# Kernel optimization log

Hardware: AMD Instinct MI355X
Metric: run time of the kernel (lower is better)

The kernel has to match this reference:

```python
import jax, jax.numpy as jnp
import numpy as np

K = 5            # srn kernel size (kernels[0])
EPSILON = 1e-3   # epsilons -> SRN additive noise scale
BN_EPS = 1e-5
NUM_SLICES = 3
OUT_CH = 64
CLASSES = 5


def _unfold(x, k):
    # torch.nn.Unfold, padding=0: (B, C*k*k, L), channel-major then (kh, kw) row-major
    B, C, H, W = x.shape
    Ho, Wo = H - k + 1, W - k + 1
    cols = jnp.stack([x[:, :, i:i + Ho, j:j + Wo]
                      for i in range(k) for j in range(k)], axis=2)  # (B,C,k*k,Ho,Wo)
    return cols.reshape(B, C * k * k, Ho * Wo), Ho, Wo


def _bn(x, g, b):
    # BatchNorm2d in training mode: batch statistics, biased variance
    m = x.mean((0, 2, 3), keepdims=True)
    v = x.var((0, 2, 3), keepdims=True)
    return (x - m) * jax.lax.rsqrt(v + BN_EPS) * g[None, :, None, None] + b[None, :, None, None]


def _conv(x, w, b):
    y = jax.lax.conv_general_dilated(x, w, (1, 1), 'VALID',
                                     dimension_numbers=('NCHW', 'OIHW', 'NCHW'))
    return y + b[None, :, None, None]


def _avgpool(x, s):
    B, C, H, W = x.shape
    return x.reshape(B, C, H // s, s, W // s, s).mean((3, 5))


def _maxpool(x, s):
    B, C, H, W = x.shape
    return x.reshape(B, C, H // s, s, W // s, s).max((3, 5))


def _srn(x, srn_w):
    B = x.shape[0]
    y, Ho, Wo = _unfold(x, K)                               # (B, n, L)
    y = y + EPSILON * jax.random.normal(jax.random.key(42), y.shape, y.dtype)
    gg = jnp.std(y, axis=1, ddof=1, keepdims=True)          # torch.std is unbiased
    y = y / gg
    O, C, _, _, S = srn_w.shape
    n = C * K * K
    X = srn_w.reshape(O, n, S)
    X = jnp.concatenate([jnp.ones((O, n, 1), X.dtype), X], axis=2)   # (O, n, S+1)
    Xcov = jnp.einsum('onf,ong->ofg', X, X)                 # X^T X, (O, 4, 4)
    Xinv = jnp.linalg.inv(Xcov)
    M = jnp.einsum('ofg,ong->ofn', Xinv, X)
    Wc = jnp.einsum('ofn,bnl->bofl', M, y)
    pred = jnp.einsum('onf,bofl->bonl', X, Wc)              # fitted values (B,O,n,L)
    err = jnp.mean((y[:, None] - pred) ** 2, axis=2)        # (B,O,L)
    err = err.reshape(B, O, Ho, Wo)
    A = (jnp.exp(-err) - np.exp(-1.0)) / (1.0 - np.exp(-1.0))
    return A - 0.5


def setup_inputs() -> dict:
    key = jax.random.key(0)
    ks = jax.random.split(key, 12)
    x = jax.random.normal(ks[0], (4, 3, 64, 64), jnp.float32)
    # xavier-style init scaled up for numerical stability of the small-matrix inverse
    srn_w = 0.05 * jax.random.normal(ks[1], (OUT_CH, 3, K, K, NUM_SLICES), jnp.float32)
    conv2_w = 0.05 * jax.random.normal(ks[2], (128, 64, 3, 3), jnp.float32)
    conv2_b = 0.01 * jax.random.normal(ks[3], (128,), jnp.float32)
    conv3_w = 0.05 * jax.random.normal(ks[4], (128, 128, 3, 3), jnp.float32)
    conv3_b = 0.01 * jax.random.normal(ks[5], (128,), jnp.float32)
    conv4_w = 0.05 * jax.random.normal(ks[6], (128, 128, 3, 3), jnp.float32)
    conv4_b = 0.01 * jax.random.normal(ks[7], (128,), jnp.float32)
    bn1_g = jnp.ones((64,), jnp.float32); bn1_b = jnp.zeros((64,), jnp.float32)
    bn2_g = jnp.ones((128,), jnp.float32); bn2_b = jnp.zeros((128,), jnp.float32)
    bn3_g = jnp.ones((128,), jnp.float32); bn3_b = jnp.zeros((128,), jnp.float32)
    bn4_g = jnp.ones((128,), jnp.float32); bn4_b = jnp.zeros((128,), jnp.float32)
    fc2_w = 0.05 * jax.random.normal(ks[8], (CLASSES, 128, 1, 1), jnp.float32)
    fc2_b = 0.01 * jax.random.normal(ks[9], (CLASSES,), jnp.float32)
    return dict(x=x, srn_w=srn_w, conv2_w=conv2_w, conv2_b=conv2_b,
                conv3_w=conv3_w, conv3_b=conv3_b, conv4_w=conv4_w, conv4_b=conv4_b,
                bn1_g=bn1_g, bn1_b=bn1_b, bn2_g=bn2_g, bn2_b=bn2_b,
                bn3_g=bn3_g, bn3_b=bn3_b, bn4_g=bn4_g, bn4_b=bn4_b,
                fc2_w=fc2_w, fc2_b=fc2_b)


def reference(x, srn_w, conv2_w, conv2_b, conv3_w, conv3_b, conv4_w, conv4_b,
              bn1_g, bn1_b, bn2_g, bn2_b, bn3_g, bn3_b, bn4_g, bn4_b,
              fc2_w, fc2_b):
    h = _srn(x, srn_w)                                      # (B,64,60,60)
    h = _avgpool(h, 2)
    h = _bn(h, bn1_g, bn1_b)
    h = jax.nn.relu(_bn(_conv(h, conv2_w, conv2_b), bn2_g, bn2_b))
    h = _avgpool(h, 2)
    h = jax.nn.relu(_bn(_conv(h, conv3_w, conv3_b), bn3_g, bn3_b))
    h = _maxpool(h, 2)
    h = jax.nn.relu(_bn(_conv(h, conv4_w, conv4_b), bn4_g, bn4_b))
    h = _maxpool(h, 4)                                      # (B,128,1,1)
    flat = h.reshape(h.shape[0], -1)                        # (B,128)
    return flat @ fc2_w.reshape(CLASSES, -1).T + fc2_b      # 1x1 conv == matmul
```

## Files before the change

kernel.cpp:

```cpp
#include <hip/hip_runtime.h>
#include <math.h>

__device__ __align__(16) float g_G[64 * 16];
__device__ __align__(16) float g_Wp[64 * 240];
__device__ __align__(16) float g_w2p[9 * 2304 * 4];
__device__ __align__(16) float g_w3p[17 * 2304 * 4];
__device__ __align__(16) float g_w4p[8 * 4608 * 4];
__device__ float g_s1[64],  g_q1[64];
__device__ float g_s2[128], g_q2[128];
__device__ float g_s3[128], g_q3[128];
__device__ float g_s4[128], g_q4[128];
__device__ __align__(16) float g_h1[4 * 30 * 30 * 64];
__device__ __align__(16) float g_h2[4 * 14 * 14 * 4 * 128];
__device__ __align__(16) float g_h3[4 * 6 * 6 * 4 * 128];
__device__ __align__(16) float g_h4[4 * 16 * 128];

__global__ void k_prep(const float* __restrict__ srn_w, const float* __restrict__ w2,
                       const float* __restrict__ w3, const float* __restrict__ w4) {
    int t = threadIdx.x, bid = blockIdx.x;
    int gid = bid * 256 + t, gstride = 128 * 256;
    for (int i = gid; i < 14400; i += gstride) {
        int o = i / 225, j = i % 225, row = j / 15, col = j % 15;
        g_Wp[o * 240 + row * 16 + col] = srn_w[i];
    }
    for (int j = gid; j < 73728; j += gstride) {
        int c = j & 3, s4 = j >> 2;
        int sl = s4 % 36, tmp = s4 / 36, oc_l = tmp & 63, blk = tmp >> 6;
        int it = blk & 3, ocg = blk >> 2;
        int kw = sl % 3, icq = (sl / 3) & 3, kh = sl / 12;
        int ic = it * 16 + icq * 4 + c;
        g_w2p[j] = w2[((ocg * 64 + oc_l) * 64 + ic) * 9 + kh * 3 + kw];
    }
    for (int j = gid; j < 147456; j += gstride) {
        int c = j & 3, s4 = j >> 2;
        int sl = s4 % 36, tmp = s4 / 36, oc_l = tmp & 63, blk = tmp >> 6;
        int it = blk & 7, ocg = blk >> 3;
        int kw = sl % 3, icq = (sl / 3) & 3, kh = sl / 12;
        int ic = it * 16 + icq * 4 + c;
        g_w3p[j] = w3[((ocg * 64 + oc_l) * 128 + ic) * 9 + kh * 3 + kw];
    }
    for (int j = gid; j < 147456; j += gstride) {
        int c = j & 3, s4 = j >> 2;
        int sl = s4 % 72, tmp = s4 / 72, oc_l = tmp & 15, blkq = tmp >> 4;
        int icq = blkq & 3, ocg = blkq >> 2;
        int kw = sl % 3, icb = (sl / 3) & 7, kh = sl / 24;
        int ic = icq * 32 + icb * 4 + c;
        g_w4p[j] = w4[((ocg * 16 + oc_l) * 128 + ic) * 9 + kh * 3 + kw];
    }
    if (bid == 0) {
        if (t < 64) { g_s1[t] = 0.f; g_q1[t] = 0.f; }
        if (t < 128) {
            g_s2[t] = 0.f; g_q2[t] = 0.f;
            g_s3[t] = 0.f; g_q3[t] = 0.f;
            g_s4[t] = 0.f; g_q4[t] = 0.f;
        }
        if (t < 64) {
            int o = t;
            const float* w = srn_w + o * 225;
            float c01 = 0, c02 = 0, c03 = 0, c11 = 0, c12 = 0, c13 = 0,
                  c22 = 0, c23 = 0, c33 = 0;
            for (int n = 0; n < 75; n++) {
                float w1 = w[n * 3 + 0], w2v = w[n * 3 + 1], w3v = w[n * 3 + 2];
                c01 += w1; c02 += w2v; c03 += w3v;
                c11 += w1 * w1; c12 += w1 * w2v; c13 += w1 * w3v;
                c22 += w2v * w2v; c23 += w2v * w3v; c33 += w3v * w3v;
            }
            float A[4][8];
            A[0][0] = 75.f; A[0][1] = c01; A[0][2] = c02; A[0][3] = c03;
            A[1][0] = c01;  A[1][1] = c11; A[1][2] = c12; A[1][3] = c13;
            A[2][0] = c02;  A[2][1] = c12; A[2][2] = c22; A[2][3] = c23;
            A[3][0] = c03;  A[3][1] = c13; A[3][2] = c23; A[3][3] = c33;
            for (int i = 0; i < 4; i++)
                for (int j = 0; j < 4; j++) A[i][4 + j] = (i == j) ? 1.f : 0.f;
            for (int p = 0; p < 4; p++) {
                float ip = 1.f / A[p][p];
                for (int j = 0; j < 8; j++) A[p][j] *= ip;
                for (int i = 0; i < 4; i++) if (i != p) {
                    float f = A[i][p];
                    for (int j = 0; j < 8; j++) A[i][j] -= f * A[p][j];
                }
            }
            for (int i = 0; i < 4; i++)
                for (int j = 0; j < 4; j++) g_G[o * 16 + i * 4 + j] = A[i][4 + j];
        }
    }
}

__global__ __launch_bounds__(256) void k_srn(const float* __restrict__ x) {
    __shared__ __align__(16) float wlds[64 * 244];
    __shared__ __align__(16) float glds[64 * 20];
    __shared__ float xsm[648];
    __shared__ float part[2 * 15 * 66];
    __shared__ float redS[256], redQ[256];
    int blk = blockIdx.x;
    int b = blk / 60, rem = blk % 60, r = rem >> 1, ch = rem & 1;
    int t = threadIdx.x;

    float4 wreg[15];
#pragma unroll
    for (int k = 0; k < 15; k++) wreg[k] = ((const float4*)g_Wp)[k * 256 + t];
    float4 greg = ((const float4*)g_G)[t];
    float xr[3];
#pragma unroll
    for (int k = 0; k < 3; k++) {
        int i = t + k * 256;
        if (i < 648) {
            int c = i / 216, rm = i % 216, rr = rm / 36, col = rm % 36;
            int gc = ch * 30 + col; if (gc > 63) gc = 63;
            xr[k] = x[((b * 3 + c) * 64 + (2 * r + rr)) * 64 + gc];
        }
    }
#pragma unroll
    for (int k = 0; k < 15; k++) {
        int idx = k * 256 + t;
        *(float4*)&wlds[(idx / 60) * 244 + (idx % 60) * 4] = wreg[k];
    }
    *(float4*)&glds[(t >> 2) * 20 + (t & 3) * 4] = greg;
#pragma unroll
    for (int k = 0; k < 3; k++) { int i = t + k * 256; if (i < 648) xsm[i] = xr[k]; }
    __syncthreads();

    int w = t >> 6, o = t & 63;
    int rw = w & 1, cq = w >> 1, base = cq * 16;

    float z1[16], z2[16], z3[16], s[16], q[16];
#pragma unroll
    for (int i = 0; i < 16; i++) { z1[i] = 0; z2[i] = 0; z3[i] = 0; s[i] = 0; q[i] = 0; }

    for (int c = 0; c < 3; c++) {
#pragma unroll
        for (int kh = 0; kh < 5; kh++) {
            float xv[20];
#pragma unroll
            for (int k = 0; k < 20; k++) xv[k] = xsm[(c * 6 + rw + kh) * 36 + base + k];
            float wf[16];
            const float* wp = &wlds[o * 244 + (c * 5 + kh) * 16];
            *(float4*)&wf[0]  = *(const float4*)&wp[0];
            *(float4*)&wf[4]  = *(const float4*)&wp[4];
            *(float4*)&wf[8]  = *(const float4*)&wp[8];
            *(float4*)&wf[12] = *(const float4*)&wp[12];
#pragma unroll
            for (int kw = 0; kw < 5; kw++) {
                float w1 = wf[kw * 3], w2 = wf[kw * 3 + 1], w3 = wf[kw * 3 + 2];
#pragma unroll
                for (int i = 0; i < 16; i++) {
                    float v = xv[kw + i];
                    s[i] += v; q[i] += v * v;
                    z1[i] += w1 * v; z2[i] += w2 * v; z3[i] += w3 * v;
                }
            }
        }
    }

    float gm[16];
    {
        const float* gp = &glds[o * 20];
        *(float4*)&gm[0]  = *(const float4*)&gp[0];
        *(float4*)&gm[4]  = *(const float4*)&gp[4];
        *(float4*)&gm[8]  = *(const float4*)&gp[8];
        *(float4*)&gm[12] = *(const float4*)&gp[12];
    }
    const float C1 = 0.36787944117144233f;
    const float INV = 1.5819767068693265f;
#pragma unroll
    for (int pp = 0; pp < 8; pp++) {
        int pl = cq * 8 + pp;
        if (pl < 15) {
            float aa = 0.f;
#pragma unroll
            for (int e = 0; e < 2; e++) {
                int i = 2 * pp + e;
                float sum = s[i], sq = q[i];
                float gg2 = (sq - sum * sum * (1.f / 75.f)) * (1.f / 74.f);
                float zf[4] = { sum, z1[i], z2[i], z3[i] };
                float qf = 0.f;
#pragma unroll
                for (int f = 0; f < 4; f++) {
                    float acc = 0.f;
#pragma unroll
                    for (int h = 0; h < 4; h++) acc += gm[f * 4 + h] * zf[h];
                    qf += acc * zf[f];
                }
                float err = (sq - qf) / (75.f * gg2);
                aa += (expf(-err) - C1) * INV - 0.5f;
            }
            part[(rw * 15 + pl) * 66 + o] = 0.25f * aa;
        }
    }
    __syncthreads();

    int j = t >> 6;
    float ps = 0.f, pq = 0.f;
    for (int pl = j; pl < 15; pl += 4) {
        float v = part[pl * 66 + o] + part[(15 + pl) * 66 + o];
        g_h1[((b * 30 + r) * 30 + ch * 15 + pl) * 64 + o] = v;
        ps += v; pq += v * v;
    }
    redS[t] = ps; redQ[t] = pq;
    __syncthreads();
    if (t < 64) {
        atomicAdd(&g_s1[t], redS[t] + redS[64 + t] + redS[128 + t] + redS[192 + t]);
        atomicAdd(&g_q1[t], redQ[t] + redQ[64 + t] + redQ[128 + t] + redQ[192 + t]);
    }
}

__global__ __launch_bounds__(256) void k_conv2(const float* __restrict__ g1,
                                               const float* __restrict__ b1) {
    __shared__ __align__(16) float ws[64 * 148];
    __shared__ __align__(16) float xs[3 * 30 * 64];
    __shared__ float redS[256], redQ[256];
    int blk = blockIdx.x;
    int b = blk / 56, rem = blk % 56, oh = rem >> 1, ocg = rem & 1;
    int t = threadIdx.x;
    int oc_l = t & 63, qtr = t >> 6, owb = qtr * 7;

    {
        int icb = (t & 15) * 4;
        float4 S = *(const float4*)&g_s1[icb], Q = *(const float4*)&g_q1[icb];
        float4 G4 = *(const float4*)&g1[icb], B4 = *(const float4*)&b1[icb];
        float scv[4], shv[4];
        float mm[4] = { S.x, S.y, S.z, S.w }, qq[4] = { Q.x, Q.y, Q.z, Q.w };
        float gg[4] = { G4.x, G4.y, G4.z, G4.w }, bb[4] = { B4.x, B4.y, B4.z, B4.w };
#pragma unroll
        for (int c = 0; c < 4; c++) {
            float m = mm[c] * (1.f / 3600.f);
            float v = qq[c] * (1.f / 3600.f) - m * m;
            scv[c] = gg[c] * rsqrtf(v + 1e-5f);
            shv[c] = bb[c] - m * scv[c];
        }
        const float4* src4 = (const float4*)(g_h1 + (b * 900 + oh * 30) * 64);
        float4 xr[6];
#pragma unroll
        for (int k = 0; k < 6; k++) { int i4 = t + k * 256; if (i4 < 1440) xr[k] = src4[i4]; }
        const float4* wsrc0 = (const float4*)g_w2p;
        float4 wreg[9];
#pragma unroll
        for (int k = 0; k < 9; k++) wreg[k] = wsrc0[(ocg * 4) * 2304 + k * 256 + t];
#pragma unroll
        for (int k = 0; k < 6; k++) {
            int i4 = t + k * 256;
            if (i4 < 1440) {
                float4 v;
                v.x = xr[k].x * scv[0] + shv[0]; v.y = xr[k].y * scv[1] + shv[1];
                v.z = xr[k].z * scv[2] + shv[2]; v.w = xr[k].w * scv[3] + shv[3];
                *(float4*)&xs[i4 * 4] = v;
            }
        }
#pragma unroll
        for (int k = 0; k < 9; k++) {
            int idx = k * 256 + t;
            *(float4*)&ws[(idx / 36) * 148 + (idx % 36) * 4] = wreg[k];
        }
    }
    __syncthreads();

    float acc[7] = {0, 0, 0, 0, 0, 0, 0};
    const float4* wsrc = (const float4*)g_w2p + (ocg * 4) * 2304;
    for (int it = 0; it < 4; ++it) {
        float4 wreg[9];
        if (it < 3) {
#pragma unroll
            for (int k = 0; k < 9; k++) wreg[k] = wsrc[(it + 1) * 2304 + k * 256 + t];
        }
#pragma unroll 1
        for (int icq = 0; icq < 4; icq++) {
            int xoff = it * 16 + icq * 4;
#pragma unroll
            for (int kh = 0; kh < 3; kh++) {
                const float* wb = &ws[oc_l * 148 + (kh * 4 + icq) * 12];
                float4 w0 = *(const float4*)&wb[0];
                float4 w1 = *(const float4*)&wb[4];
                float4 w2v = *(const float4*)&wb[8];
                const float* xrow = &xs[(kh * 30 + owb) * 64 + xoff];
                float4 x0 = *(const float4*)&xrow[0];
                float4 x1 = *(const float4*)&xrow[64];
#pragma unroll
                for (int i = 0; i < 7; i++) {
                    float4 x2 = *(const float4*)&xrow[(i + 2) * 64];
                    acc[i] += w0.x * x0.x + w0.y * x0.y + w0.z * x0.z + w0.w * x0.w
                            + w1.x * x1.x + w1.y * x1.y + w1.z * x1.z + w1.w * x1.w
                            + w2v.x * x2.x + w2v.y * x2.y + w2v.z * x2.z + w2v.w * x2.w;
                    x0 = x1; x1 = x2;
                }
            }
        }
        if (it < 3) {
            __syncthreads();
#pragma unroll
            for (int k = 0; k < 9; k++) {
                int idx = k * 256 + t;
                *(float4*)&ws[(idx / 36) * 148 + (idx % 36) * 4] = wreg[k];
            }
            __syncthreads();
        }
    }
    int oc = ocg * 64 + oc_l;
    float ps = 0.f, pq = 0.f;
#pragma unroll
    for (int i = 0; i < 7; i++) {
        int ow = owb + i;
        g_h2[(((b * 14 + (oh >> 1)) * 14 + (ow >> 1)) * 4 + (oh & 1) * 2 + (ow & 1)) * 128 + oc] = acc[i];
        ps += acc[i]; pq += acc[i] * acc[i];
    }
    redS[t] = ps; redQ[t] = pq;
    __syncthreads();
    if (t < 64) {
        atomicAdd(&g_s2[ocg * 64 + t], redS[t] + redS[64 + t] + redS[128 + t] + redS[192 + t]);
        atomicAdd(&g_q2[ocg * 64 + t], redQ[t] + redQ[64 + t] + redQ[128 + t] + redQ[192 + t]);
    }
}

__global__ __launch_bounds__(256) void k_conv3(const float* __restrict__ g2,
                                               const float* __restrict__ b2) {
    __shared__ __align__(16) float ws[64 * 148];
    __shared__ __align__(16) float xs[3 * 14 * 128];
    __shared__ float redS[256], redQ[256];
    int blk = blockIdx.x;
    int b = blk / 24, rem = blk % 24, oh = rem >> 1, ocg = rem & 1;
    int t = threadIdx.x;
    int oc_l = t & 63, qtr = t >> 6, owb = qtr * 3;

    {
        int icb = (t & 31) * 4;
        float4 S = *(const float4*)&g_s2[icb], Q = *(const float4*)&g_q2[icb];
        float4 G4 = *(const float4*)&g2[icb], B4 = *(const float4*)&b2[icb];
        float scv[4], shv[4];
        float mm[4] = { S.x, S.y, S.z, S.w }, qq[4] = { Q.x, Q.y, Q.z, Q.w };
        float gg[4] = { G4.x, G4.y, G4.z, G4.w }, bb[4] = { B4.x, B4.y, B4.z, B4.w };
#pragma unroll
        for (int c = 0; c < 4; c++) {
            float m = mm[c] * (1.f / 3136.f);
            float v = qq[c] * (1.f / 3136.f) - m * m;
            scv[c] = gg[c] * rsqrtf(v + 1e-5f);
            shv[c] = bb[c] - m * scv[c];
        }
        const float4* wsrc0 = (const float4*)g_w3p;
        float4 wreg[9];
#pragma unroll
        for (int k = 0; k < 9; k++) wreg[k] = wsrc0[(ocg * 8) * 2304 + k * 256 + t];
        float4 va[6], vb[6], vc[6], vd[6];
#pragma unroll
        for (int k = 0; k < 6; k++) {
            int i4 = t + k * 256;
            if (i4 < 1344) {
                int px = (i4 >> 5) % 14, rr = i4 / 448;
                const float4* p0 = (const float4*)&g_h2[(((b * 14 + oh + rr) * 14 + px) * 4) * 128 + (i4 & 31) * 4];
                va[k] = p0[0]; vb[k] = p0[32]; vc[k] = p0[64]; vd[k] = p0[96];
            }
        }
#pragma unroll
        for (int k = 0; k < 9; k++) {
            int idx = k * 256 + t;
            *(float4*)&ws[(idx / 36) * 148 + (idx % 36) * 4] = wreg[k];
        }
#pragma unroll
        for (int k = 0; k < 6; k++) {
            int i4 = t + k * 256;
            if (i4 < 1344) {
                float4 o4;
                o4.x = 0.25f * (fmaxf(va[k].x * scv[0] + shv[0], 0.f) + fmaxf(vb[k].x * scv[0] + shv[0], 0.f)
                              + fmaxf(vc[k].x * scv[0] + shv[0], 0.f) + fmaxf(vd[k].x * scv[0] + shv[0], 0.f));
                o4.y = 0.25f * (fmaxf(va[k].y * scv[1] + shv[1], 0.f) + fmaxf(vb[k].y * scv[1] + shv[1], 0.f)
                              + fmaxf(vc[k].y * scv[1] + shv[1], 0.f) + fmaxf(vd[k].y * scv[1] + shv[1], 0.f));
                o4.z = 0.25f * (fmaxf(va[k].z * scv[2] + shv[2], 0.f) + fmaxf(vb[k].z * scv[2] + shv[2], 0.f)
                              + fmaxf(vc[k].z * scv[2] + shv[2], 0.f) + fmaxf(vd[k].z * scv[2] + shv[2], 0.f));
                o4.w = 0.25f * (fmaxf(va[k].w * scv[3] + shv[3], 0.f) + fmaxf(vb[k].w * scv[3] + shv[3], 0.f)
                              + fmaxf(vc[k].w * scv[3] + shv[3], 0.f) + fmaxf(vd[k].w * scv[3] + shv[3], 0.f));
                *(float4*)&xs[i4 * 4] = o4;
            }
        }
    }
    __syncthreads();

    float acc[3] = {0, 0, 0};
    const float4* wsrc = (const float4*)g_w3p + (ocg * 8) * 2304;
    for (int it = 0; it < 8; ++it) {
        float4 wreg[9];
        if (it < 7) {
#pragma unroll
            for (int k = 0; k < 9; k++) wreg[k] = wsrc[(it + 1) * 2304 + k * 256 + t];
        }
#pragma unroll 1
        for (int icq = 0; icq < 4; icq++) {
            int xoff = it * 16 + icq * 4;
#pragma unroll
            for (int kh = 0; kh < 3; kh++) {
                const float* wb = &ws[oc_l * 148 + (kh * 4 + icq) * 12];
                float4 w0 = *(const float4*)&wb[0];
                float4 w1 = *(const float4*)&wb[4];
                float4 w2v = *(const float4*)&wb[8];
                const float* xrow = &xs[(kh * 14 + owb) * 128 + xoff];
                float4 x0 = *(const float4*)&xrow[0];
                float4 x1 = *(const float4*)&xrow[128];
#pragma unroll
                for (int i = 0; i < 3; i++) {
                    float4 x2 = *(const float4*)&xrow[(i + 2) * 128];
                    acc[i] += w0.x * x0.x + w0.y * x0.y + w0.z * x0.z + w0.w * x0.w
                            + w1.x * x1.x + w1.y * x1.y + w1.z * x1.z + w1.w * x1.w
                            + w2v.x * x2.x + w2v.y * x2.y + w2v.z * x2.z + w2v.w * x2.w;
                    x0 = x1; x1 = x2;
                }
            }
        }
        if (it < 7) {
            __syncthreads();
#pragma unroll
            for (int k = 0; k < 9; k++) {
                int idx = k * 256 + t;
                *(float4*)&ws[(idx / 36) * 148 + (idx % 36) * 4] = wreg[k];
            }
            __syncthreads();
        }
    }
    int oc = ocg * 64 + oc_l;
    float ps = 0.f, pq = 0.f;
#pragma unroll
    for (int i = 0; i < 3; i++) {
        int ow = owb + i;
        g_h3[(((b * 6 + (oh >> 1)) * 6 + (ow >> 1)) * 4 + (oh & 1) * 2 + (ow & 1)) * 128 + oc] = acc[i];
        ps += acc[i]; pq += acc[i] * acc[i];
    }
    redS[t] = ps; redQ[t] = pq;
    __syncthreads();
    if (t < 64) {
        atomicAdd(&g_s3[ocg * 64 + t], redS[t] + redS[64 + t] + redS[128 + t] + redS[192 + t]);
        atomicAdd(&g_q3[ocg * 64 + t], redQ[t] + redQ[64 + t] + redQ[128 + t] + redQ[192 + t]);
    }
}

__global__ __launch_bounds__(256) void k_conv4(const float* __restrict__ g3,
                                               const float* __restrict__ b3) {
    __shared__ __align__(16) float ws[64 * 292];
    __shared__ __align__(16) float xs[3 * 6 * 128];
    __shared__ float red[256];
    int blk = blockIdx.x;
    int b = blk / 32, rem = blk % 32, oh = rem / 8, ocg = rem % 8;
    int t = threadIdx.x;
    int oc_l = t & 15, ow = (t >> 4) & 3, icq = t >> 6;

    {
        int icb = (t & 31) * 4;
        float4 S = *(const float4*)&g_s3[icb], Q = *(const float4*)&g_q3[icb];
        float4 G4 = *(const float4*)&g3[icb], B4 = *(const float4*)&b3[icb];
        float scv[4], shv[4];
        float mm[4] = { S.x, S.y, S.z, S.w }, qq[4] = { Q.x, Q.y, Q.z, Q.w };
        float gg[4] = { G4.x, G4.y, G4.z, G4.w }, bb[4] = { B4.x, B4.y, B4.z, B4.w };
#pragma unroll
        for (int c = 0; c < 4; c++) {
            float m = mm[c] * (1.f / 576.f);
            float v = qq[c] * (1.f / 576.f) - m * m;
            scv[c] = gg[c] * rsqrtf(v + 1e-5f);
            shv[c] = bb[c] - m * scv[c];
        }
        const float4* wsrc = (const float4*)g_w4p + ocg * 4608;
        float4 wreg[18];
#pragma unroll
        for (int k = 0; k < 18; k++) wreg[k] = wsrc[k * 256 + t];
        float4 va[3], vb[3], vc[3], vd[3];
#pragma unroll
        for (int k = 0; k < 3; k++) {
            int i4 = t + k * 256;
            if (i4 < 576) {
                int px = (i4 >> 5) % 6, rr = i4 / 192;
                const float4* p0 = (const float4*)&g_h3[(((b * 6 + oh + rr) * 6 + px) * 4) * 128 + (i4 & 31) * 4];
                va[k] = p0[0]; vb[k] = p0[32]; vc[k] = p0[64]; vd[k] = p0[96];
            }
        }
#pragma unroll
        for (int k = 0; k < 18; k++) {
            int idx = k * 256 + t;
            *(float4*)&ws[(idx / 72) * 292 + (idx % 72) * 4] = wreg[k];
        }
#pragma unroll
        for (int k = 0; k < 3; k++) {
            int i4 = t + k * 256;
            if (i4 < 576) {
                float4 o4;
                o4.x = fmaxf(fmaxf(fmaxf(va[k].x * scv[0] + shv[0], vb[k].x * scv[0] + shv[0]),
                                   fmaxf(vc[k].x * scv[0] + shv[0], vd[k].x * scv[0] + shv[0])), 0.f);
                o4.y = fmaxf(fmaxf(fmaxf(va[k].y * scv[1] + shv[1], vb[k].y * scv[1] + shv[1]),
                                   fmaxf(vc[k].y * scv[1] + shv[1], vd[k].y * scv[1] + shv[1])), 0.f);
                o4.z = fmaxf(fmaxf(fmaxf(va[k].z * scv[2] + shv[2], vb[k].z * scv[2] + shv[2]),
                                   fmaxf(vc[k].z * scv[2] + shv[2], vd[k].z * scv[2] + shv[2])), 0.f);
                o4.w = fmaxf(fmaxf(fmaxf(va[k].w * scv[3] + shv[3], vb[k].w * scv[3] + shv[3]),
                                   fmaxf(vc[k].w * scv[3] + shv[3], vd[k].w * scv[3] + shv[3])), 0.f);
                *(float4*)&xs[i4 * 4] = o4;
            }
        }
    }
    __syncthreads();

    float acc = 0.f;
    const float* wbase = &ws[(icq * 16 + oc_l) * 292];
#pragma unroll 1
    for (int icbq = 0; icbq < 8; icbq++) {
#pragma unroll
        for (int kh = 0; kh < 3; kh++) {
            const float* wb = &wbase[(kh * 8 + icbq) * 12];
            float4 w0 = *(const float4*)&wb[0];
            float4 w1 = *(const float4*)&wb[4];
            float4 w2v = *(const float4*)&wb[8];
            float4 x0 = *(const float4*)&xs[(kh * 6 + ow) * 128 + icq * 32 + icbq * 4];
            float4 x1 = *(const float4*)&xs[(kh * 6 + ow + 1) * 128 + icq * 32 + icbq * 4];
            float4 x2 = *(const float4*)&xs[(kh * 6 + ow + 2) * 128 + icq * 32 + icbq * 4];
            acc += w0.x * x0.x + w0.y * x0.y + w0.z * x0.z + w0.w * x0.w
                 + w1.x * x1.x + w1.y * x1.y + w1.z * x1.z + w1.w * x1.w
                 + w2v.x * x2.x + w2v.y * x2.y + w2v.z * x2.z + w2v.w * x2.w;
        }
    }
    red[t] = acc;
    __syncthreads();
    if (t < 64) {
        float v = red[t] + red[t + 64] + red[t + 128] + red[t + 192];
        int oc = ocg * 16 + (t & 15);
        g_h4[((b * 4 + oh) * 4 + (t >> 4)) * 128 + oc] = v;
        float ps = v + __shfl_xor(v, 16);  ps += __shfl_xor(ps, 32);
        float pv = v * v;
        float pq = pv + __shfl_xor(pv, 16); pq += __shfl_xor(pq, 32);
        if (t < 16) { atomicAdd(&g_s4[ocg * 16 + t], ps); atomicAdd(&g_q4[ocg * 16 + t], pq); }
    }
}

__global__ __launch_bounds__(256) void k_final(const float* __restrict__ g4,
                                               const float* __restrict__ b4,
                                               const float* __restrict__ fcw,
                                               const float* __restrict__ fcb,
                                               float* __restrict__ out) {
    __shared__ float sc[128], sh[128];
    __shared__ float pooled[4][128];
    int t = threadIdx.x;
    if (t < 128) {
        float m = g_s4[t] * (1.f / 64.f);
        float v = g_q4[t] * (1.f / 64.f) - m * m;
        float rs = rsqrtf(v + 1e-5f);
        sc[t] = g4[t] * rs; sh[t] = b4[t] - m * sc[t];
    }
    __syncthreads();
    for (int item = t; item < 512; item += 256) {
        int b = item >> 7, oc = item & 127;
        float s = sc[oc], h = sh[oc];
        float mx = 0.f;
#pragma unroll
        for (int k = 0; k < 16; k++) mx = fmaxf(mx, g_h4[(b * 16 + k) * 128 + oc] * s + h);
        pooled[b][oc] = mx;
    }
    __syncthreads();
    if (t < 20) {
        int b = t / 5, cls = t % 5;
        float acc = fcb[cls];
        const float* w = &fcw[cls * 128];
        for (int oc = 0; oc < 128; oc++) acc += pooled[b][oc] * w[oc];
        out[b * 5 + cls] = acc;
    }
}

extern "C" void kernel_launch(void* const* d_in, const int* in_sizes, int n_in,
                              void* d_out, int out_size, void* d_ws, size_t ws_size,
                              hipStream_t stream) {
    (void)in_sizes; (void)n_in; (void)out_size; (void)d_ws; (void)ws_size;
    const float* x     = (const float*)d_in[0];
    const float* srn_w = (const float*)d_in[1];
    const float* w2    = (const float*)d_in[2];
    const float* w3    = (const float*)d_in[4];
    const float* w4    = (const float*)d_in[6];
    const float* g1 = (const float*)d_in[8];  const float* b1 = (const float*)d_in[9];
    const float* g2 = (const float*)d_in[10]; const float* b2 = (const float*)d_in[11];
    const float* g3 = (const float*)d_in[12]; const float* b3 = (const float*)d_in[13];
    const float* g4 = (const float*)d_in[14]; const float* b4 = (const float*)d_in[15];
    const float* fcw = (const float*)d_in[16]; const float* fcb = (const float*)d_in[17];
    float* out = (float*)d_out;

    k_prep <<<dim3(128), dim3(256), 0, stream>>>(srn_w, w2, w3, w4);
    k_srn  <<<dim3(240), dim3(256), 0, stream>>>(x);
    k_conv2<<<dim3(224), dim3(256), 0, stream>>>(g1, b1);
    k_conv3<<<dim3(96),  dim3(256), 0, stream>>>(g2, b2);
    k_conv4<<<dim3(128), dim3(256), 0, stream>>>(g3, b3);
    k_final<<<dim3(1),   dim3(256), 0, stream>>>(g4, b4, fcw, fcb, out);
}
```

Baseline: 115.4 us.

## Fuse all stages into one persistent kernel with software grid barriers

Replaces the six separate launches (prep, srn, conv2, conv3, conv4, final) with a single persistent kernel of 240 blocks that separates the stages with an atomic-counter grid barrier. The SRN stage now streams weights one input channel at a time through a smaller LDS buffer so shared memory fits the fused kernel's dynamic allocation. The aim is to remove kernel launch gaps and tail effects between small stages. In exchange, each barrier adds a global atomic round trip. Correctness depends on all 240 blocks being co-resident, and the stages that use fewer blocks leave the rest idle at the barrier.

```diff
diff --git a/kernel.cpp b/kernel.cpp
--- a/kernel.cpp
+++ b/kernel.cpp
@@ -1,5 +1,7 @@
 #include <hip/hip_runtime.h>
 #include <math.h>
+
+#define GRID 240
 
 __device__ __align__(16) float g_G[64 * 16];
 __device__ __align__(16) float g_Wp[64 * 240];
@@ -14,47 +16,77 @@
 __device__ __align__(16) float g_h2[4 * 14 * 14 * 4 * 128];
 __device__ __align__(16) float g_h3[4 * 6 * 6 * 4 * 128];
 __device__ __align__(16) float g_h4[4 * 16 * 128];
-
-__global__ void k_prep(const float* __restrict__ srn_w, const float* __restrict__ w2,
-                       const float* __restrict__ w3, const float* __restrict__ w4) {
-    int t = threadIdx.x, bid = blockIdx.x;
-    int gid = bid * 256 + t, gstride = 128 * 256;
-    for (int i = gid; i < 14400; i += gstride) {
-        int o = i / 225, j = i % 225, row = j / 15, col = j % 15;
-        g_Wp[o * 240 + row * 16 + col] = srn_w[i];
+__device__ int g_cnt;
+__device__ int g_gen;
+
+__device__ __forceinline__ void gridbar() {
+    __syncthreads();
+    __threadfence();
+    if (threadIdx.x == 0) {
+        int gen = __hip_atomic_load(&g_gen, __ATOMIC_RELAXED, __HIP_MEMORY_SCOPE_AGENT);
+        if (__hip_atomic_fetch_add(&g_cnt, 1, __ATOMIC_ACQ_REL, __HIP_MEMORY_SCOPE_AGENT)
+            == (int)gridDim.x - 1) {
+            __hip_atomic_store(&g_cnt, 0, __ATOMIC_RELAXED, __HIP_MEMORY_SCOPE_AGENT);
+            __hip_atomic_store(&g_gen, gen + 1, __ATOMIC_RELEASE, __HIP_MEMORY_SCOPE_AGENT);
+        } else {
+            while (__hip_atomic_load(&g_gen, __ATOMIC_RELAXED, __HIP_MEMORY_SCOPE_AGENT) == gen)
+                __builtin_amdgcn_s_sleep(2);
+        }
     }
-    for (int j = gid; j < 73728; j += gstride) {
-        int c = j & 3, s4 = j >> 2;
-        int sl = s4 % 36, tmp = s4 / 36, oc_l = tmp & 63, blk = tmp >> 6;
-        int it = blk & 3, ocg = blk >> 2;
-        int kw = sl % 3, icq = (sl / 3) & 3, kh = sl / 12;
-        int ic = it * 16 + icq * 4 + c;
-        g_w2p[j] = w2[((ocg * 64 + oc_l) * 64 + ic) * 9 + kh * 3 + kw];
-    }
-    for (int j = gid; j < 147456; j += gstride) {
-        int c = j & 3, s4 = j >> 2;
-        int sl = s4 % 36, tmp = s4 / 36, oc_l = tmp & 63, blk = tmp >> 6;
-        int it = blk & 7, ocg = blk >> 3;
-        int kw = sl % 3, icq = (sl / 3) & 3, kh = sl / 12;
-        int ic = it * 16 + icq * 4 + c;
-        g_w3p[j] = w3[((ocg * 64 + oc_l) * 128 + ic) * 9 + kh * 3 + kw];
-    }
-    for (int j = gid; j < 147456; j += gstride) {
-        int c = j & 3, s4 = j >> 2;
-        int sl = s4 % 72, tmp = s4 / 72, oc_l = tmp & 15, blkq = tmp >> 4;
-        int icq = blkq & 3, ocg = blkq >> 2;
-        int kw = sl % 3, icb = (sl / 3) & 7, kh = sl / 24;
-        int ic = icq * 32 + icb * 4 + c;
-        g_w4p[j] = w4[((ocg * 16 + oc_l) * 128 + ic) * 9 + kh * 3 + kw];
-    }
-    if (bid == 0) {
-        if (t < 64) { g_s1[t] = 0.f; g_q1[t] = 0.f; }
-        if (t < 128) {
+    __syncthreads();
+    __threadfence();
+}
+
+extern "C" __global__ void __launch_bounds__(256)
+k_fused(const float* __restrict__ x, const float* __restrict__ srn_w,
+        const float* __restrict__ w2, const float* __restrict__ w3,
+        const float* __restrict__ w4,
+        const float* __restrict__ g1, const float* __restrict__ b1,
+        const float* __restrict__ g2, const float* __restrict__ b2,
+        const float* __restrict__ g3, const float* __restrict__ b3,
+        const float* __restrict__ g4, const float* __restrict__ b4,
+        const float* __restrict__ fcw, const float* __restrict__ fcb,
+        float* __restrict__ out) {
+    extern __shared__ __align__(16) float smem[];
+    int bid = blockIdx.x, t = threadIdx.x;
+
+    {
+        int gid = bid * 256 + t, gstride = GRID * 256;
+        for (int i = gid; i < 14400; i += gstride) {
+            int o = i / 225, j = i % 225, row = j / 15, col = j % 15;
+            g_Wp[o * 240 + row * 16 + col] = srn_w[i];
+        }
+        for (int j = gid; j < 73728; j += gstride) {
+            int c = j & 3, s4 = j >> 2;
+            int sl = s4 % 36, tmp = s4 / 36, oc_l = tmp & 63, blk = tmp >> 6;
+            int it = blk & 3, ocg = blk >> 2;
+            int kw = sl % 3, icq = (sl / 3) & 3, kh = sl / 12;
+            int ic = it * 16 + icq * 4 + c;
+            g_w2p[j] = w2[((ocg * 64 + oc_l) * 64 + ic) * 9 + kh * 3 + kw];
+        }
+        for (int j = gid; j < 147456; j += gstride) {
+            int c = j & 3, s4 = j >> 2;
+            int sl = s4 % 36, tmp = s4 / 36, oc_l = tmp & 63, blk = tmp >> 6;
+            int it = blk & 7, ocg = blk >> 3;
+            int kw = sl % 3, icq = (sl / 3) & 3, kh = sl / 12;
+            int ic = it * 16 + icq * 4 + c;
+            g_w3p[j] = w3[((ocg * 64 + oc_l) * 128 + ic) * 9 + kh * 3 + kw];
+        }
+        for (int j = gid; j < 147456; j += gstride) {
+            int c = j & 3, s4 = j >> 2;
+            int sl = s4 % 72, tmp = s4 / 72, oc_l = tmp & 15, blkq = tmp >> 4;
+            int icq = blkq & 3, ocg = blkq >> 2;
+            int kw = sl % 3, icb = (sl / 3) & 7, kh = sl / 24;
+            int ic = icq * 32 + icb * 4 + c;
+            g_w4p[j] = w4[((ocg * 16 + oc_l) * 128 + ic) * 9 + kh * 3 + kw];
+        }
+        if (bid == 1 && t < 128) {
+            if (t < 64) { g_s1[t] = 0.f; g_q1[t] = 0.f; }
             g_s2[t] = 0.f; g_q2[t] = 0.f;
             g_s3[t] = 0.f; g_q3[t] = 0.f;
             g_s4[t] = 0.f; g_q4[t] = 0.f;
         }
-        if (t < 64) {
+        if (bid == 0 && t < 64) {
             int o = t;
             const float* w = srn_w + o * 225;
             float c01 = 0, c02 = 0, c03 = 0, c11 = 0, c12 = 0, c13 = 0,
@@ -84,473 +116,490 @@
                 for (int j = 0; j < 4; j++) g_G[o * 16 + i * 4 + j] = A[i][4 + j];
         }
     }
-}
-
-__global__ __launch_bounds__(256) void k_srn(const float* __restrict__ x) {
-    __shared__ __align__(16) float wlds[64 * 244];
-    __shared__ __align__(16) float glds[64 * 20];
-    __shared__ float xsm[648];
-    __shared__ float part[2 * 15 * 66];
-    __shared__ float redS[256], redQ[256];
-    int blk = blockIdx.x;
-    int b = blk / 60, rem = blk % 60, r = rem >> 1, ch = rem & 1;
-    int t = threadIdx.x;
-
-    float4 wreg[15];
-#pragma unroll
-    for (int k = 0; k < 15; k++) wreg[k] = ((const float4*)g_Wp)[k * 256 + t];
-    float4 greg = ((const float4*)g_G)[t];
-    float xr[3];
-#pragma unroll
-    for (int k = 0; k < 3; k++) {
-        int i = t + k * 256;
-        if (i < 648) {
-            int c = i / 216, rm = i % 216, rr = rm / 36, col = rm % 36;
-            int gc = ch * 30 + col; if (gc > 63) gc = 63;
-            xr[k] = x[((b * 3 + c) * 64 + (2 * r + rr)) * 64 + gc];
+    gridbar();
+
+    {
+        float* wl   = smem;
+        float* gl   = smem + 5376;
+        float* xsm  = smem + 6656;
+        float* part = smem + 7304;
+        float* redS = smem + 9284;
+        float* redQ = smem + 9540;
+        int b = bid / 60, rem = bid % 60, r = rem >> 1, ch = rem & 1;
+
+        float4 greg = ((const float4*)g_G)[t];
+        float xr[3];
+#pragma unroll
+        for (int k = 0; k < 3; k++) {
+            int i = t + k * 256;
+            if (i < 648) {
+                int c = i / 216, rm = i % 216, rr = rm / 36, col = rm % 36;
+                int gc = ch * 30 + col; if (gc > 63) gc = 63;
+                xr[k] = x[((b * 3 + c) * 64 + (2 * r + rr)) * 64 + gc];
+            }
+        }
+        float4 wreg[5];
+#pragma unroll
+        for (int k = 0; k < 5; k++) {
+            int idx = k * 256 + t;
+            wreg[k] = ((const float4*)g_Wp)[(idx / 20) * 60 + 0 * 20 + (idx % 20)];
+        }
+        *(float4*)&gl[(t >> 2) * 20 + (t & 3) * 4] = greg;
+#pragma unroll
+        for (int k = 0; k < 3; k++) { int i = t + k * 256; if (i < 648) xsm[i] = xr[k]; }
+#pragma unroll
+        for (int k = 0; k < 5; k++) {
+            int idx = k * 256 + t;
+            *(float4*)&wl[(idx / 20) * 84 + (idx % 20) * 4] = wreg[k];
+        }
+        __syncthreads();
+
+        int w = t >> 6, o = t & 63;
+        int rw = w & 1, cq = w >> 1, base = cq * 16;
+
+        float z1[16], z2[16], z3[16], s[16], q[16];
+#pragma unroll
+        for (int i = 0; i < 16; i++) { z1[i]=0; z2[i]=0; z3[i]=0; s[i]=0; q[i]=0; }
+
+        for (int c = 0; c < 3; c++) {
+            if (c < 2) {
+#pragma unroll
+                for (int k = 0; k < 5; k++) {
+                    int idx = k * 256 + t;
+                    wreg[k] = ((const float4*)g_Wp)[(idx / 20) * 60 + (c + 1) * 20 + (idx % 20)];
+                }
+            }
+#pragma unroll
+            for (int kh = 0; kh < 5; kh++) {
+                float xv[20];
+#pragma unroll
+                for (int k = 0; k < 20; k++) xv[k] = xsm[(c * 6 + rw + kh) * 36 + base + k];
+                float wf[16];
+                const float* wp = &wl[o * 84 + kh * 16];
+                *(float4*)&wf[0]  = *(const float4*)&wp[0];
+                *(float4*)&wf[4]  = *(const float4*)&wp[4];
+                *(float4*)&wf[8]  = *(const float4*)&wp[8];
+                *(float4*)&wf[12] = *(const float4*)&wp[12];
+#pragma unroll
+                for (int kw = 0; kw < 5; kw++) {
+                    float w1 = wf[kw * 3], w2v = wf[kw * 3 + 1], w3v = wf[kw * 3 + 2];
+#pragma unroll
+                    for (int i = 0; i < 16; i++) {
+                        float v = xv[kw + i];
+                        s[i] += v; q[i] += v * v;
+                        z1[i] += w1 * v; z2[i] += w2v * v; z3[i] += w3v * v;
+                    }
+                }
+            }
+            if (c < 2) {
+                __syncthreads();
+#pragma unroll
+                for (int k = 0; k < 5; k++) {
+                    int idx = k * 256 + t;
+                    *(float4*)&wl[(idx / 20) * 84 + (idx % 20) * 4] = wreg[k];
+                }
+                __syncthreads();
+            }
+        }
+
+        float gm[16];
+        {
+            const float* gp = &gl[o * 20];
+            *(float4*)&gm[0]  = *(const float4*)&gp[0];
+            *(float4*)&gm[4]  = *(const float4*)&gp[4];
+            *(float4*)&gm[8]  = *(const float4*)&gp[8];
+            *(float4*)&gm[12] = *(const float4*)&gp[12];
+        }
+        const float C1 = 0.36787944117144233f;
+        const float INV = 1.5819767068693265f;
+#pragma unroll
+        for (int pp = 0; pp < 8; pp++) {
+            int pl = cq * 8 + pp;
+            if (pl < 15) {
+                float aa = 0.f;
+#pragma unroll
+                for (int e = 0; e < 2; e++) {
+                    int i = 2 * pp + e;
+                    float sum = s[i], sq = q[i];
+                    float gg2 = (sq - sum * sum * (1.f / 75.f)) * (1.f / 74.f);
+                    float zf[4] = { sum, z1[i], z2[i], z3[i] };
+                    float qf = 0.f;
+#pragma unroll
+                    for (int f = 0; f < 4; f++) {
+                        float acc = 0.f;
+#pragma unroll
+                        for (int h = 0; h < 4; h++) acc += gm[f * 4 + h] * zf[h];
+                        qf += acc * zf[f];
+                    }
+                    float err = (sq - qf) / (75.f * gg2);
+                    aa += (expf(-err) - C1) * INV - 0.5f;
+                }
+                part[(rw * 15 + pl) * 66 + o] = 0.25f * aa;
+            }
+        }
+        __syncthreads();
+
+        int j = t >> 6;
+        float ps = 0.f, pq = 0.f;
+        for (int pl = j; pl < 15; pl += 4) {
+            float v = part[pl * 66 + o] + part[(15 + pl) * 66 + o];
+            g_h1[((b * 30 + r) * 30 + ch * 15 + pl) * 64 + o] = v;
+            ps += v; pq += v * v;
+        }
+        redS[t] = ps; redQ[t] = pq;
+        __syncthreads();
+        if (t < 64) {
+            atomicAdd(&g_s1[t], redS[t] + redS[64 + t] + redS[128 + t] + redS[192 + t]);
+            atomicAdd(&g_q1[t], redQ[t] + redQ[64 + t] + redQ[128 + t] + redQ[192 + t]);
         }
     }
-#pragma unroll
-    for (int k = 0; k < 15; k++) {
-        int idx = k * 256 + t;
-        *(float4*)&wlds[(idx / 60) * 244 + (idx % 60) * 4] = wreg[k];
-    }
-    *(float4*)&glds[(t >> 2) * 20 + (t & 3) * 4] = greg;
-#pragma unroll
-    for (int k = 0; k < 3; k++) { int i = t + k * 256; if (i < 648) xsm[i] = xr[k]; }
-    __syncthreads();
-
-    int w = t >> 6, o = t & 63;
-    int rw = w & 1, cq = w >> 1, base = cq * 16;
-
-    float z1[16], z2[16], z3[16], s[16], q[16];
-#pragma unroll
-    for (int i = 0; i < 16; i++) { z1[i] = 0; z2[i] = 0; z3[i] = 0; s[i] = 0; q[i] = 0; }
-
-    for (int c = 0; c < 3; c++) {
-#pragma unroll
-        for (int kh = 0; kh < 5; kh++) {
-            float xv[20];
-#pragma unroll
-            for (int k = 0; k < 20; k++) xv[k] = xsm[(c * 6 + rw + kh) * 36 + base + k];
-            float wf[16];
-            const float* wp = &wlds[o * 244 + (c * 5 + kh) * 16];
-            *(float4*)&wf[0]  = *(const float4*)&wp[0];
-            *(float4*)&wf[4]  = *(const float4*)&wp[4];
-            *(float4*)&wf[8]  = *(const float4*)&wp[8];
-            *(float4*)&wf[12] = *(const float4*)&wp[12];
-#pragma unroll
-            for (int kw = 0; kw < 5; kw++) {
-                float w1 = wf[kw * 3], w2 = wf[kw * 3 + 1], w3 = wf[kw * 3 + 2];
-#pragma unroll
-                for (int i = 0; i < 16; i++) {
-                    float v = xv[kw + i];
-                    s[i] += v; q[i] += v * v;
-                    z1[i] += w1 * v; z2[i] += w2 * v; z3[i] += w3 * v;
-                }
-            }
-        }
-    }
-
-    float gm[16];
-    {
-        const float* gp = &glds[o * 20];
-        *(float4*)&gm[0]  = *(const float4*)&gp[0];
-        *(float4*)&gm[4]  = *(const float4*)&gp[4];
-        *(float4*)&gm[8]  = *(const float4*)&gp[8];
-        *(float4*)&gm[12] = *(const float4*)&gp[12];
-    }
-    const float C1 = 0.36787944117144233f;
-    const float INV = 1.5819767068693265f;
-#pragma unroll
-    for (int pp = 0; pp < 8; pp++) {
-        int pl = cq * 8 + pp;
-        if (pl < 15) {
-            float aa = 0.f;
-#pragma unroll
-            for (int e = 0; e < 2; e++) {
-                int i = 2 * pp + e;
-                float sum = s[i], sq = q[i];
-                float gg2 = (sq - sum * sum * (1.f / 75.f)) * (1.f / 74.f);
-                float zf[4] = { sum, z1[i], z2[i], z3[i] };
-                float qf = 0.f;
-#pragma unroll
-                for (int f = 0; f < 4; f++) {
-                    float acc = 0.f;
-#pragma unroll
-                    for (int h = 0; h < 4; h++) acc += gm[f * 4 + h] * zf[h];
-                    qf += acc * zf[f];
-                }
-                float err = (sq - qf) / (75.f * gg2);
-                aa += (expf(-err) - C1) * INV - 0.5f;
-            }
-            part[(rw * 15 + pl) * 66 + o] = 0.25f * aa;
-        }
-    }
-    __syncthreads();
-
-    int j = t >> 6;
-    float ps = 0.f, pq = 0.f;
-    for (int pl = j; pl < 15; pl += 4) {
-        float v = part[pl * 66 + o] + part[(15 + pl) * 66 + o];
-        g_h1[((b * 30 + r) * 30 + ch * 15 + pl) * 64 + o] = v;
-        ps += v; pq += v * v;
-    }
-    redS[t] = ps; redQ[t] = pq;
-    __syncthreads();
-    if (t < 64) {
-        atomicAdd(&g_s1[t], redS[t] + redS[64 + t] + redS[128 + t] + redS[192 + t]);
-        atomicAdd(&g_q1[t], redQ[t] + redQ[64 + t] + redQ[128 + t] + redQ[192 + t]);
-    }
-}
-
-__global__ __launch_bounds__(256) void k_conv2(const float* __restrict__ g1,
-                                               const float* __restrict__ b1) {
-    __shared__ __align__(16) float ws[64 * 148];
-    __shared__ __align__(16) float xs[3 * 30 * 64];
-    __shared__ float redS[256], redQ[256];
-    int blk = blockIdx.x;
-    int b = blk / 56, rem = blk % 56, oh = rem >> 1, ocg = rem & 1;
-    int t = threadIdx.x;
-    int oc_l = t & 63, qtr = t >> 6, owb = qtr * 7;
-
-    {
-        int icb = (t & 15) * 4;
-        float4 S = *(const float4*)&g_s1[icb], Q = *(const float4*)&g_q1[icb];
-        float4 G4 = *(const float4*)&g1[icb], B4 = *(const float4*)&b1[icb];
-        float scv[4], shv[4];
-        float mm[4] = { S.x, S.y, S.z, S.w }, qq[4] = { Q.x, Q.y, Q.z, Q.w };
-        float gg[4] = { G4.x, G4.y, G4.z, G4.w }, bb[4] = { B4.x, B4.y, B4.z, B4.w };
-#pragma unroll
-        for (int c = 0; c < 4; c++) {
-            float m = mm[c] * (1.f / 3600.f);
-            float v = qq[c] * (1.f / 3600.f) - m * m;
-            scv[c] = gg[c] * rsqrtf(v + 1e-5f);
-            shv[c] = bb[c] - m * scv[c];
-        }
-        const float4* src4 = (const float4*)(g_h1 + (b * 900 + oh * 30) * 64);
-        float4 xr[6];
-#pragma unroll
-        for (int k = 0; k < 6; k++) { int i4 = t + k * 256; if (i4 < 1440) xr[k] = src4[i4]; }
-        const float4* wsrc0 = (const float4*)g_w2p;
-        float4 wreg[9];
-#pragma unroll
-        for (int k = 0; k < 9; k++) wreg[k] = wsrc0[(ocg * 4) * 2304 + k * 256 + t];
-#pragma unroll
-        for (int k = 0; k < 6; k++) {
-            int i4 = t + k * 256;
-            if (i4 < 1440) {
-                float4 v;
-                v.x = xr[k].x * scv[0] + shv[0]; v.y = xr[k].y * scv[1] + shv[1];
-                v.z = xr[k].z * scv[2] + shv[2]; v.w = xr[k].w * scv[3] + shv[3];
-                *(float4*)&xs[i4 * 4] = v;
-            }
-        }
-#pragma unroll
-        for (int k = 0; k < 9; k++) {
-            int idx = k * 256 + t;
-            *(float4*)&ws[(idx / 36) * 148 + (idx % 36) * 4] = wreg[k];
-        }
-    }
-    __syncthreads();
-
-    float acc[7] = {0, 0, 0, 0, 0, 0, 0};
-    const float4* wsrc = (const float4*)g_w2p + (ocg * 4) * 2304;
-    for (int it = 0; it < 4; ++it) {
-        float4 wreg[9];
-        if (it < 3) {
-#pragma unroll
-            for (int k = 0; k < 9; k++) wreg[k] = wsrc[(it + 1) * 2304 + k * 256 + t];
-        }
-#pragma unroll 1
-        for (int icq = 0; icq < 4; icq++) {
-            int xoff = it * 16 + icq * 4;
-#pragma unroll
-            for (int kh = 0; kh < 3; kh++) {
-                const float* wb = &ws[oc_l * 148 + (kh * 4 + icq) * 12];
-                float4 w0 = *(const float4*)&wb[0];
-                float4 w1 = *(const float4*)&wb[4];
-                float4 w2v = *(const float4*)&wb[8];
-                const float* xrow = &xs[(kh * 30 + owb) * 64 + xoff];
-                float4 x0 = *(const float4*)&xrow[0];
-                float4 x1 = *(const float4*)&xrow[64];
-#pragma unroll
-                for (int i = 0; i < 7; i++) {
-                    float4 x2 = *(const float4*)&xrow[(i + 2) * 64];
-                    acc[i] += w0.x * x0.x + w0.y * x0.y + w0.z * x0.z + w0.w * x0.w
-                            + w1.x * x1.x + w1.y * x1.y + w1.z * x1.z + w1.w * x1.w
-                            + w2v.x * x2.x + w2v.y * x2.y + w2v.z * x2.z + w2v.w * x2.w;
-                    x0 = x1; x1 = x2;
-                }
-            }
-        }
-        if (it < 3) {
-            __syncthreads();
+    gridbar();
+
+    if (bid < 224) {
+        float* ws   = smem;
+        float* xs   = smem + 9472;
+        float* redS = smem + 15232;
+        float* redQ = smem + 15488;
+        int b = bid / 56, rem = bid % 56, oh = rem >> 1, ocg = rem & 1;
+        int oc_l = t & 63, qtr = t >> 6, owb = qtr * 7;
+
+        {
+            int icb = (t & 15) * 4;
+            float4 S = *(const float4*)&g_s1[icb], Q = *(const float4*)&g_q1[icb];
+            float4 G4 = *(const float4*)&g1[icb], B4 = *(const float4*)&b1[icb];
+            float scv[4], shv[4];
+            float mm[4] = { S.x, S.y, S.z, S.w }, qq[4] = { Q.x, Q.y, Q.z, Q.w };
+            float gg[4] = { G4.x, G4.y, G4.z, G4.w }, bb[4] = { B4.x, B4.y, B4.z, B4.w };
+#pragma unroll
+            for (int c = 0; c < 4; c++) {
+                float m = mm[c] * (1.f / 3600.f);
+                float v = qq[c] * (1.f / 3600.f) - m * m;
+                scv[c] = gg[c] * rsqrtf(v + 1e-5f);
+                shv[c] = bb[c] - m * scv[c];
+            }
+            const float4* src4 = (const float4*)(g_h1 + (b * 900 + oh * 30) * 64);
+            float4 xr[6];
+#pragma unroll
+            for (int k = 0; k < 6; k++) { int i4 = t + k * 256; if (i4 < 1440) xr[k] = src4[i4]; }
+            const float4* wsrc0 = (const float4*)g_w2p;
+            float4 wreg[9];
+#pragma unroll
+            for (int k = 0; k < 9; k++) wreg[k] = wsrc0[(ocg * 4) * 2304 + k * 256 + t];
+#pragma unroll
+            for (int k = 0; k < 6; k++) {
+                int i4 = t + k * 256;
+                if (i4 < 1440) {
+                    float4 v;
+                    v.x = xr[k].x * scv[0] + shv[0]; v.y = xr[k].y * scv[1] + shv[1];
+                    v.z = xr[k].z * scv[2] + shv[2]; v.w = xr[k].w * scv[3] + shv[3];
+                    *(float4*)&xs[i4 * 4] = v;
+                }
+            }
 #pragma unroll
             for (int k = 0; k < 9; k++) {
                 int idx = k * 256 + t;
                 *(float4*)&ws[(idx / 36) * 148 + (idx % 36) * 4] = wreg[k];
             }
-            __syncthreads();
+        }
+        __syncthreads();
+
+        float acc[7] = {0, 0, 0, 0, 0, 0, 0};
+        const float4* wsrc = (const float4*)g_w2p + (ocg * 4) * 2304;
+        for (int it = 0; it < 4; ++it) {
+            float4 wreg[9];
+            if (it < 3) {
+#pragma unroll
+                for (int k = 0; k < 9; k++) wreg[k] = wsrc[(it + 1) * 2304 + k * 256 + t];
+            }
+#pragma unroll 1
+            for (int icq = 0; icq < 4; icq++) {
+                int xoff = it * 16 + icq * 4;
+#pragma unroll
+                for (int kh = 0; kh < 3; kh++) {
+                    const float* wb = &ws[oc_l * 148 + (kh * 4 + icq) * 12];
+                    float4 w0 = *(const float4*)&wb[0];
+                    float4 w1 = *(const float4*)&wb[4];
+                    float4 w2v = *(const float4*)&wb[8];
+                    const float* xrow = &xs[(kh * 30 + owb) * 64 + xoff];
+                    float4 x0 = *(const float4*)&xrow[0];
+                    float4 x1 = *(const float4*)&xrow[64];
+#pragma unroll
+                    for (int i = 0; i < 7; i++) {
+                        float4 x2 = *(const float4*)&xrow[(i + 2) * 64];
+                        acc[i] += w0.x * x0.x + w0.y * x0.y + w0.z * x0.z + w0.w * x0.w
+                                + w1.x * x1.x + w1.y * x1.y + w1.z * x1.z + w1.w * x1.w
+                                + w2v.x * x2.x + w2v.y * x2.y + w2v.z * x2.z + w2v.w * x2.w;
+                        x0 = x1; x1 = x2;
+                    }
+                }
+            }
+            if (it < 3) {
+                __syncthreads();
+#pragma unroll
+                for (int k = 0; k < 9; k++) {
+                    int idx = k * 256 + t;
+                    *(float4*)&ws[(idx / 36) * 148 + (idx % 36) * 4] = wreg[k];
+                }
+                __syncthreads();
+            }
+        }
+        int oc = ocg * 64 + oc_l;
+        float ps = 0.f, pq = 0.f;
+#pragma unroll
+        for (int i = 0; i < 7; i++) {
+            int ow = owb + i;
+            g_h2[(((b * 14 + (oh >> 1)) * 14 + (ow >> 1)) * 4 + (oh & 1) * 2 + (ow & 1)) * 128 + oc] = acc[i];
+            ps += acc[i]; pq += acc[i] * acc[i];
+        }
+        redS[t] = ps; redQ[t] = pq;
+        __syncthreads();
+        if (t < 64) {
+            atomicAdd(&g_s2[ocg * 64 + t], redS[t] + redS[64 + t] + redS[128 + t] + redS[192 + t]);
+            atomicAdd(&g_q2[ocg * 64 + t], redQ[t] + redQ[64 + t] + redQ[128 + t] + redQ[192 + t]);
         }
     }
-    int oc = ocg * 64 + oc_l;
-    float ps = 0.f, pq = 0.f;
-#pragma unroll
-    for (int i = 0; i < 7; i++) {
-        int ow = owb + i;
-        g_h2[(((b * 14 + (oh >> 1)) * 14 + (ow >> 1)) * 4 + (oh & 1) * 2 + (ow & 1)) * 128 + oc] = acc[i];
-        ps += acc[i]; pq += acc[i] * acc[i];
-    }
-    redS[t] = ps; redQ[t] = pq;
-    __syncthreads();
-    if (t < 64) {
-        atomicAdd(&g_s2[ocg * 64 + t], redS[t] + redS[64 + t] + redS[128 + t] + redS[192 + t]);
-        atomicAdd(&g_q2[ocg * 64 + t], redQ[t] + redQ[64 + t] + redQ[128 + t] + redQ[192 + t]);
-    }
-}
-
-__global__ __launch_bounds__(256) void k_conv3(const float* __restrict__ g2,
-                                               const float* __restrict__ b2) {
-    __shared__ __align__(16) float ws[64 * 148];
-    __shared__ __align__(16) float xs[3 * 14 * 128];
-    __shared__ float redS[256], redQ[256];
-    int blk = blockIdx.x;
-    int b = blk / 24, rem = blk % 24, oh = rem >> 1, ocg = rem & 1;
-    int t = threadIdx.x;
-    int oc_l = t & 63, qtr = t >> 6, owb = qtr * 3;
-
-    {
-        int icb = (t & 31) * 4;
-        float4 S = *(const float4*)&g_s2[icb], Q = *(const float4*)&g_q2[icb];
-        float4 G4 = *(const float4*)&g2[icb], B4 = *(const float4*)&b2[icb];
-        float scv[4], shv[4];
-        float mm[4] = { S.x, S.y, S.z, S.w }, qq[4] = { Q.x, Q.y, Q.z, Q.w };
-        float gg[4] = { G4.x, G4.y, G4.z, G4.w }, bb[4] = { B4.x, B4.y, B4.z, B4.w };
-#pragma unroll
-        for (int c = 0; c < 4; c++) {
-            float m = mm[c] * (1.f / 3136.f);
-            float v = qq[c] * (1.f / 3136.f) - m * m;
-            scv[c] = gg[c] * rsqrtf(v + 1e-5f);
-            shv[c] = bb[c] - m * scv[c];
-        }
-        const float4* wsrc0 = (const float4*)g_w3p;
-        float4 wreg[9];
-#pragma unroll
-        for (int k = 0; k < 9; k++) wreg[k] = wsrc0[(ocg * 8) * 2304 + k * 256 + t];
-        float4 va[6], vb[6], vc[6], vd[6];
-#pragma unroll
-        for (int k = 0; k < 6; k++) {
-            int i4 = t + k * 256;
-            if (i4 < 1344) {
-                int px = (i4 >> 5) % 14, rr = i4 / 448;
-                const float4* p0 = (const float4*)&g_h2[(((b * 14 + oh + rr) * 14 + px) * 4) * 128 + (i4 & 31) * 4];
-                va[k] = p0[0]; vb[k] = p0[32]; vc[k] = p0[64]; vd[k] = p0[96];
-            }
-        }
-#pragma unroll
-        for (int k = 0; k < 9; k++) {
-            int idx = k * 256 + t;
-            *(float4*)&ws[(idx / 36) * 148 + (idx % 36) * 4] = wreg[k];
-        }
-#pragma unroll
-        for (int k = 0; k < 6; k++) {
-            int i4 = t + k * 256;
-            if (i4 < 1344) {
-                float4 o4;
-                o4.x = 0.25f * (fmaxf(va[k].x * scv[0] + shv[0], 0.f) + fmaxf(vb[k].x * scv[0] + shv[0], 0.f)
-                              + fmaxf(vc[k].x * scv[0] + shv[0], 0.f) + fmaxf(vd[k].x * scv[0] + shv[0], 0.f));
-                o4.y = 0.25f * (fmaxf(va[k].y * scv[1] + shv[1], 0.f) + fmaxf(vb[k].y * scv[1] + shv[1], 0.f)
-                              + fmaxf(vc[k].y * scv[1] + shv[1], 0.f) + fmaxf(vd[k].y * scv[1] + shv[1], 0.f));
-                o4.z = 0.25f * (fmaxf(va[k].z * scv[2] + shv[2], 0.f) + fmaxf(vb[k].z * scv[2] + shv[2], 0.f)
-                              + fmaxf(vc[k].z * scv[2] + shv[2], 0.f) + fmaxf(vd[k].z * scv[2] + shv[2], 0.f));
-                o4.w = 0.25f * (fmaxf(va[k].w * scv[3] + shv[3], 0.f) + fmaxf(vb[k].w * scv[3] + shv[3], 0.f)
-                              + fmaxf(vc[k].w * scv[3] + shv[3], 0.f) + fmaxf(vd[k].w * scv[3] + shv[3], 0.f));
-                *(float4*)&xs[i4 * 4] = o4;
-            }
-        }
-    }
-    __syncthreads();
-
-    float acc[3] = {0, 0, 0};
-    const float4* wsrc = (const float4*)g_w3p + (ocg * 8) * 2304;
-    for (int it = 0; it < 8; ++it) {
-        float4 wreg[9];
-        if (it < 7) {
-#pragma unroll
-            for (int k = 0; k < 9; k++) wreg[k] = wsrc[(it + 1) * 2304 + k * 256 + t];
-        }
-#pragma unroll 1
-        for (int icq = 0; icq < 4; icq++) {
-            int xoff = it * 16 + icq * 4;
-#pragma unroll
-            for (int kh = 0; kh < 3; kh++) {
-                const float* wb = &ws[oc_l * 148 + (kh * 4 + icq) * 12];
-                float4 w0 = *(const float4*)&wb[0];
-                float4 w1 = *(const float4*)&wb[4];
-                float4 w2v = *(const float4*)&wb[8];
-                const float* xrow = &xs[(kh * 14 + owb) * 128 + xoff];
-                float4 x0 = *(const float4*)&xrow[0];
-                float4 x1 = *(const float4*)&xrow[128];
-#pragma unroll
-                for (int i = 0; i < 3; i++) {
-                    float4 x2 = *(const float4*)&xrow[(i + 2) * 128];
-                    acc[i] += w0.x * x0.x + w0.y * x0.y + w0.z * x0.z + w0.w * x0.w
-                            + w1.x * x1.x + w1.y * x1.y + w1.z * x1.z + w1.w * x1.w
-                            + w2v.x * x2.x + w2v.y * x2.y + w2v.z * x2.z + w2v.w * x2.w;
-                    x0 = x1; x1 = x2;
-                }
-            }
-        }
-        if (it < 7) {
-            __syncthreads();
+    gridbar();
+
+    if (bid < 96) {
+        float* ws   = smem;
+        float* xs   = smem + 9472;
+        float* redS = smem + 14848;
+        float* redQ = smem + 15104;
+        int b = bid / 24, rem = bid % 24, oh = rem >> 1, ocg = rem & 1;
+        int oc_l = t & 63, qtr = t >> 6, owb = qtr * 3;
+
+        {
+            int icb = (t & 31) * 4;
+            float4 S = *(const float4*)&g_s2[icb], Q = *(const float4*)&g_q2[icb];
+            float4 G4 = *(const float4*)&g2[icb], B4 = *(const float4*)&b2[icb];
+            float scv[4], shv[4];
+            float mm[4] = { S.x, S.y, S.z, S.w }, qq[4] = { Q.x, Q.y, Q.z, Q.w };
+            float gg[4] = { G4.x, G4.y, G4.z, G4.w }, bb[4] = { B4.x, B4.y, B4.z, B4.w };
+#pragma unroll
+            for (int c = 0; c < 4; c++) {
+                float m = mm[c] * (1.f / 3136.f);
+                float v = qq[c] * (1.f / 3136.f) - m * m;
+                scv[c] = gg[c] * rsqrtf(v + 1e-5f);
+                shv[c] = bb[c] - m * scv[c];
+            }
+            const float4* wsrc0 = (const float4*)g_w3p;
+            float4 wreg[9];
+#pragma unroll
+            for (int k = 0; k < 9; k++) wreg[k] = wsrc0[(ocg * 8) * 2304 + k * 256 + t];
+            float4 pa[6], pb[6], pc[6], pd[6];
+#pragma unroll
+            for (int k = 0; k < 6; k++) {
+                int i4 = t + k * 256;
+                if (i4 < 1344) {
+                    int px = (i4 >> 5) % 14, rr = i4 / 448;
+                    const float4* p0 = (const float4*)&g_h2[(((b * 14 + oh + rr) * 14 + px) * 4) * 128 + (i4 & 31) * 4];
+                    pa[k] = p0[0]; pb[k] = p0[32]; pc[k] = p0[64]; pd[k] = p0[96];
+                }
+            }
 #pragma unroll
             for (int k = 0; k < 9; k++) {
                 int idx = k * 256 + t;
                 *(float4*)&ws[(idx / 36) * 148 + (idx % 36) * 4] = wreg[k];
             }
+#pragma unroll
+            for (int k = 0; k < 6; k++) {
+                int i4 = t + k * 256;
+                if (i4 < 1344) {
+                    float4 o4;
+                    o4.x = 0.25f * (fmaxf(pa[k].x * scv[0] + shv[0], 0.f) + fmaxf(pb[k].x * scv[0] + shv[0], 0.f)
+                                  + fmaxf(pc[k].x * scv[0] + shv[0], 0.f) + fmaxf(pd[k].x * scv[0] + shv[0], 0.f));
+                    o4.y = 0.25f * (fmaxf(pa[k].y * scv[1] + shv[1], 0.f) + fmaxf(pb[k].y * scv[1] + shv[1], 0.f)
+                                  + fmaxf(pc[k].y * scv[1] + shv[1], 0.f) + fmaxf(pd[k].y * scv[1] + shv[1], 0.f));
+                    o4.z = 0.25f * (fmaxf(pa[k].z * scv[2] + shv[2], 0.f) + fmaxf(pb[k].z * scv[2] + shv[2], 0.f)
+                                  + fmaxf(pc[k].z * scv[2] + shv[2], 0.f) + fmaxf(pd[k].z * scv[2] + shv[2], 0.f));
+                    o4.w = 0.25f * (fmaxf(pa[k].w * scv[3] + shv[3], 0.f) + fmaxf(pb[k].w * scv[3] + shv[3], 0.f)
+                                  + fmaxf(pc[k].w * scv[3] + shv[3], 0.f) + fmaxf(pd[k].w * scv[3] + shv[3], 0.f));
+                    *(float4*)&xs[i4 * 4] = o4;
+                }
+            }
+        }
+        __syncthreads();
+
+        float acc[3] = {0, 0, 0};
+        const float4* wsrc = (const float4*)g_w3p + (ocg * 8) * 2304;
+        for (int it = 0; it < 8; ++it) {
+            float4 wreg[9];
+            if (it < 7) {
+#pragma unroll
+                for (int k = 0; k < 9; k++) wreg[k] = wsrc[(it + 1) * 2304 + k * 256 + t];
+            }
+#pragma unroll 1
+            for (int icq = 0; icq < 4; icq++) {
+                int xoff = it * 16 + icq * 4;
+#pragma unroll
+                for (int kh = 0; kh < 3; kh++) {
+                    const float* wb = &ws[oc_l * 148 + (kh * 4 + icq) * 12];
+                    float4 w0 = *(const float4*)&wb[0];
+                    float4 w1 = *(const float4*)&wb[4];
+                    float4 w2v = *(const float4*)&wb[8];
+                    const float* xrow = &xs[(kh * 14 + owb) * 128 + xoff];
+                    float4 x0 = *(const float4*)&xrow[0];
+                    float4 x1 = *(const float4*)&xrow[128];
+#pragma unroll
+                    for (int i = 0; i < 3; i++) {
+                        float4 x2 = *(const float4*)&xrow[(i + 2) * 128];
+                        acc[i] += w0.x * x0.x + w0.y * x0.y + w0.z * x0.z + w0.w * x0.w
+                                + w1.x * x1.x + w1.y * x1.y + w1.z * x1.z + w1.w * x1.w
+                                + w2v.x * x2.x + w2v.y * x2.y + w2v.z * x2.z + w2v.w * x2.w;
+                        x0 = x1; x1 = x2;
+                    }
+                }
+            }
+            if (it < 7) {
+                __syncthreads();
+#pragma unroll
+                for (int k = 0; k < 9; k++) {
+                    int idx = k * 256 + t;
+                    *(float4*)&ws[(idx / 36) * 148 + (idx % 36) * 4] = wreg[k];
+                }
+                __syncthreads();
+            }
+        }
+        int oc = ocg * 64 + oc_l;
+        float ps = 0.f, pq = 0.f;
+#pragma unroll
+        for (int i = 0; i < 3; i++) {
+            int ow = owb + i;
+            g_h3[(((b * 6 + (oh >> 1)) * 6 + (ow >> 1)) * 4 + (oh & 1) * 2 + (ow & 1)) * 128 + oc] = acc[i];
+            ps += acc[i]; pq += acc[i] * acc[i];
+        }
+        redS[t] = ps; redQ[t] = pq;
+        __syncthreads();
+        if (t < 64) {
+            atomicAdd(&g_s3[ocg * 64 + t], redS[t] + redS[64 + t] + redS[128 + t] + redS[192 + t]);
+            atomicAdd(&g_q3[ocg * 64 + t], redQ[t] + redQ[64 + t] + redQ[128 + t] + redQ[192 + t]);
+        }
+    }
+    gridbar();
+
+    if (bid < 128) {
+        float* ws  = smem;
+        float* xs  = smem + 9344;
+        float* red = smem + 11648;
+        int b = bid / 32, rem = bid % 32, oh = rem / 8, ocg = rem % 8;
+        int oc_l = t & 15, ow = (t >> 4) & 3, icq = t >> 6;
+
+        {
+            int icb = (t & 31) * 4;
+            float4 S = *(const float4*)&g_s3[icb], Q = *(const float4*)&g_q3[icb];
+            float4 G4 = *(const float4*)&g3[icb], B4 = *(const float4*)&b3[icb];
+            float scv[4], shv[4];
+            float mm[4] = { S.x, S.y, S.z, S.w }, qq[4] = { Q.x, Q.y, Q.z, Q.w };
+            float gg[4] = { G4.x, G4.y, G4.z, G4.w }, bb[4] = { B4.x, B4.y, B4.z, B4.w };
+#pragma unroll
+            for (int c = 0; c < 4; c++) {
+                float m = mm[c] * (1.f / 576.f);
+                float v = qq[c] * (1.f / 576.f) - m * m;
+                scv[c] = gg[c] * rsqrtf(v + 1e-5f);
+                shv[c] = bb[c] - m * scv[c];
+            }
+            float4 pa[3], pb[3], pc[3], pd[3];
+#pragma unroll
+            for (int k = 0; k < 3; k++) {
+                int i4 = t + k * 256;
+                if (i4 < 576) {
+                    int px = (i4 >> 5) % 6, rr = i4 / 192;
+                    const float4* p0 = (const float4*)&g_h3[(((b * 6 + oh + rr) * 6 + px) * 4) * 128 + (i4 & 31) * 4];
+                    pa[k] = p0[0]; pb[k] = p0[32]; pc[k] = p0[64]; pd[k] = p0[96];
+                }
+            }
+#pragma unroll
+            for (int k = 0; k < 3; k++) {
+                int i4 = t + k * 256;
+                if (i4 < 576) {
+                    float4 o4;
+                    o4.x = fmaxf(fmaxf(fmaxf(pa[k].x * scv[0] + shv[0], pb[k].x * scv[0] + shv[0]),
+                                       fmaxf(pc[k].x * scv[0] + shv[0], pd[k].x * scv[0] + shv[0])), 0.f);
+                    o4.y = fmaxf(fmaxf(fmaxf(pa[k].y * scv[1] + shv[1], pb[k].y * scv[1] + shv[1]),
+                                       fmaxf(pc[k].y * scv[1] + shv[1], pd[k].y * scv[1] + shv[1])), 0.f);
+                    o4.z = fmaxf(fmaxf(fmaxf(pa[k].z * scv[2] + shv[2], pb[k].z * scv[2] + shv[2]),
+                                       fmaxf(pc[k].z * scv[2] + shv[2], pd[k].z * scv[2] + shv[2])), 0.f);
+                    o4.w = fmaxf(fmaxf(fmaxf(pa[k].w * scv[3] + shv[3], pb[k].w * scv[3] + shv[3]),
+                                       fmaxf(pc[k].w * scv[3] + shv[3], pd[k].w * scv[3] + shv[3])), 0.f);
+                    *(float4*)&xs[i4 * 4] = o4;
+                }
+            }
+        }
+
+        float acc = 0.f;
+        const float4* wsrc = (const float4*)g_w4p + ocg * 4608;
+        for (int h = 0; h < 2; h++) {
+            float4 wreg[9];
+#pragma unroll
+            for (int k = 0; k < 9; k++) wreg[k] = wsrc[h * 2304 + k * 256 + t];
             __syncthreads();
+#pragma unroll
+            for (int k = 0; k < 9; k++) {
+                int idx = k * 256 + t;
+                *(float4*)&ws[(idx / 72) * 292 + (idx % 72) * 4] = wreg[k];
+            }
+            __syncthreads();
+            if ((icq >> 1) == h) {
+                const float* wbase = &ws[((icq & 1) * 16 + oc_l) * 292];
+#pragma unroll 1
+                for (int icbq = 0; icbq < 8; icbq++) {
+#pragma unroll
+                    for (int kh = 0; kh < 3; kh++) {
+                        const float* wb = &wbase[(kh * 8 + icbq) * 12];
+                        float4 w0 = *(const float4*)&wb[0];
+                        float4 w1 = *(const float4*)&wb[4];
+                        float4 w2v = *(const float4*)&wb[8];
+                        float4 x0 = *(const float4*)&xs[(kh * 6 + ow) * 128 + icq * 32 + icbq * 4];
+                        float4 x1 = *(const float4*)&xs[(kh * 6 + ow + 1) * 128 + icq * 32 + icbq * 4];
+                        float4 x2 = *(const float4*)&xs[(kh * 6 + ow + 2) * 128 + icq * 32 + icbq * 4];
+                        acc += w0.x * x0.x + w0.y * x0.y + w0.z * x0.z + w0.w * x0.w
+                             + w1.x * x1.x + w1.y * x1.y + w1.z * x1.z + w1.w * x1.w
+                             + w2v.x * x2.x + w2v.y * x2.y + w2v.z * x2.z + w2v.w * x2.w;
+                    }
+                }
+            }
+        }
+        red[t] = acc;
+        __syncthreads();
+        if (t < 64) {
+            float v = red[t] + red[t + 64] + red[t + 128] + red[t + 192];
+            int oc = ocg * 16 + (t & 15);
+            g_h4[((b * 4 + oh) * 4 + (t >> 4)) * 128 + oc] = v;
+            float ps = v + __shfl_xor(v, 16);  ps += __shfl_xor(ps, 32);
+            float pv = v * v;
+            float pq = pv + __shfl_xor(pv, 16); pq += __shfl_xor(pq, 32);
+            if (t < 16) { atomicAdd(&g_s4[ocg * 16 + t], ps); atomicAdd(&g_q4[ocg * 16 + t], pq); }
         }
     }
-    int oc = ocg * 64 + oc_l;
-    float ps = 0.f, pq = 0.f;
-#pragma unroll
-    for (int i = 0; i < 3; i++) {
-        int ow = owb + i;
-        g_h3[(((b * 6 + (oh >> 1)) * 6 + (ow >> 1)) * 4 + (oh & 1) * 2 + (ow & 1)) * 128 + oc] = acc[i];
-        ps += acc[i]; pq += acc[i] * acc[i];
-    }
-    redS[t] = ps; redQ[t] = pq;
-    __syncthreads();
-    if (t < 64) {
-        atomicAdd(&g_s3[ocg * 64 + t], redS[t] + redS[64 + t] + redS[128 + t] + redS[192 + t]);
-        atomicAdd(&g_q3[ocg * 64 + t], redQ[t] + redQ[64 + t] + redQ[128 + t] + redQ[192 + t]);
-    }
-}
-
-__global__ __launch_bounds__(256) void k_conv4(const float* __restrict__ g3,
-                                               const float* __restrict__ b3) {
-    __shared__ __align__(16) float ws[64 * 292];
-    __shared__ __align__(16) float xs[3 * 6 * 128];
-    __shared__ float red[256];
-    int blk = blockIdx.x;
-    int b = blk / 32, rem = blk % 32, oh = rem / 8, ocg = rem % 8;
-    int t = threadIdx.x;
-    int oc_l = t & 15, ow = (t >> 4) & 3, icq = t >> 6;
-
-    {
-        int icb = (t & 31) * 4;
-        float4 S = *(const float4*)&g_s3[icb], Q = *(const float4*)&g_q3[icb];
-        float4 G4 = *(const float4*)&g3[icb], B4 = *(const float4*)&b3[icb];
-        float scv[4], shv[4];
-        float mm[4] = { S.x, S.y, S.z, S.w }, qq[4] = { Q.x, Q.y, Q.z, Q.w };
-        float gg[4] = { G4.x, G4.y, G4.z, G4.w }, bb[4] = { B4.x, B4.y, B4.z, B4.w };
-#pragma unroll
-        for (int c = 0; c < 4; c++) {
-            float m = mm[c] * (1.f / 576.f);
-            float v = qq[c] * (1.f / 576.f) - m * m;
-            scv[c] = gg[c] * rsqrtf(v + 1e-5f);
-            shv[c] = bb[c] - m * scv[c];
-        }
-        const float4* wsrc = (const float4*)g_w4p + ocg * 4608;
-        float4 wreg[18];
-#pragma unroll
-        for (int k = 0; k < 18; k++) wreg[k] = wsrc[k * 256 + t];
-        float4 va[3], vb[3], vc[3], vd[3];
-#pragma unroll
-        for (int k = 0; k < 3; k++) {
-            int i4 = t + k * 256;
-            if (i4 < 576) {
-                int px = (i4 >> 5) % 6, rr = i4 / 192;
-                const float4* p0 = (const float4*)&g_h3[(((b * 6 + oh + rr) * 6 + px) * 4) * 128 + (i4 & 31) * 4];
-                va[k] = p0[0]; vb[k] = p0[32]; vc[k] = p0[64]; vd[k] = p0[96];
-            }
-        }
-#pragma unroll
-        for (int k = 0; k < 18; k++) {
-            int idx = k * 256 + t;
-            *(float4*)&ws[(idx / 72) * 292 + (idx % 72) * 4] = wreg[k];
-        }
-#pragma unroll
-        for (int k = 0; k < 3; k++) {
-            int i4 = t + k * 256;
-            if (i4 < 576) {
-                float4 o4;
-                o4.x = fmaxf(fmaxf(fmaxf(va[k].x * scv[0] + shv[0], vb[k].x * scv[0] + shv[0]),
-                                   fmaxf(vc[k].x * scv[0] + shv[0], vd[k].x * scv[0] + shv[0])), 0.f);
-                o4.y = fmaxf(fmaxf(fmaxf(va[k].y * scv[1] + shv[1], vb[k].y * scv[1] + shv[1]),
-                                   fmaxf(vc[k].y * scv[1] + shv[1], vd[k].y * scv[1] + shv[1])), 0.f);
-                o4.z = fmaxf(fmaxf(fmaxf(va[k].z * scv[2] + shv[2], vb[k].z * scv[2] + shv[2]),
-                                   fmaxf(vc[k].z * scv[2] + shv[2], vd[k].z * scv[2] + shv[2])), 0.f);
-                o4.w = fmaxf(fmaxf(fmaxf(va[k].w * scv[3] + shv[3], vb[k].w * scv[3] + shv[3]),
-                                   fmaxf(vc[k].w * scv[3] + shv[3], vd[k].w * scv[3] + shv[3])), 0.f);
-                *(float4*)&xs[i4 * 4] = o4;
-            }
-        }
-    }
-    __syncthreads();
-
-    float acc = 0.f;
-    const float* wbase = &ws[(icq * 16 + oc_l) * 292];
-#pragma unroll 1
-    for (int icbq = 0; icbq < 8; icbq++) {
-#pragma unroll
-        for (int kh = 0; kh < 3; kh++) {
-            const float* wb = &wbase[(kh * 8 + icbq) * 12];
-            float4 w0 = *(const float4*)&wb[0];
-            float4 w1 = *(const float4*)&wb[4];
-            float4 w2v = *(const float4*)&wb[8];
-            float4 x0 = *(const float4*)&xs[(kh * 6 + ow) * 128 + icq * 32 + icbq * 4];
-            float4 x1 = *(const float4*)&xs[(kh * 6 + ow + 1) * 128 + icq * 32 + icbq * 4];
-            float4 x2 = *(const float4*)&xs[(kh * 6 + ow + 2) * 128 + icq * 32 + icbq * 4];
-            acc += w0.x * x0.x + w0.y * x0.y + w0.z * x0.z + w0.w * x0.w
-                 + w1.x * x1.x + w1.y * x1.y + w1.z * x1.z + w1.w * x1.w
-                 + w2v.x * x2.x + w2v.y * x2.y + w2v.z * x2.z + w2v.w * x2.w;
-        }
-    }
-    red[t] = acc;
-    __syncthreads();
-    if (t < 64) {
-        float v = red[t] + red[t + 64] + red[t + 128] + red[t + 192];
-        int oc = ocg * 16 + (t & 15);
-        g_h4[((b * 4 + oh) * 4 + (t >> 4)) * 128 + oc] = v;
-        float ps = v + __shfl_xor(v, 16);  ps += __shfl_xor(ps, 32);
-        float pv = v * v;
-        float pq = pv + __shfl_xor(pv, 16); pq += __shfl_xor(pq, 32);
-        if (t < 16) { atomicAdd(&g_s4[ocg * 16 + t], ps); atomicAdd(&g_q4[ocg * 16 + t], pq); }
-    }
-}
-
-__global__ __launch_bounds__(256) void k_final(const float* __restrict__ g4,
-                                               const float* __restrict__ b4,
-                                               const float* __restrict__ fcw,
-                                               const float* __restrict__ fcb,
-                                               float* __restrict__ out) {
-    __shared__ float sc[128], sh[128];
-    __shared__ float pooled[4][128];
-    int t = threadIdx.x;
-    if (t < 128) {
-        float m = g_s4[t] * (1.f / 64.f);
-        float v = g_q4[t] * (1.f / 64.f) - m * m;
-        float rs = rsqrtf(v + 1e-5f);
-        sc[t] = g4[t] * rs; sh[t] = b4[t] - m * sc[t];
-    }
-    __syncthreads();
-    for (int item = t; item < 512; item += 256) {
-        int b = item >> 7, oc = item & 127;
-        float s = sc[oc], h = sh[oc];
-        float mx = 0.f;
-#pragma unroll
-        for (int k = 0; k < 16; k++) mx = fmaxf(mx, g_h4[(b * 16 + k) * 128 + oc] * s + h);
-        pooled[b][oc] = mx;
-    }
-    __syncthreads();
-    if (t < 20) {
-        int b = t / 5, cls = t % 5;
-        float acc = fcb[cls];
-        const float* w = &fcw[cls * 128];
-        for (int oc = 0; oc < 128; oc++) acc += pooled[b][oc] * w[oc];
-        out[b * 5 + cls] = acc;
+    gridbar();
+
+    if (bid == 0) {
+        float* sc = smem;
+        float* sh = smem + 128;
+        float* pooled = smem + 256;
+        if (t < 128) {
+            float m = g_s4[t] * (1.f / 64.f);
+            float v = g_q4[t] * (1.f / 64.f) - m * m;
+            float rs = rsqrtf(v + 1e-5f);
+            sc[t] = g4[t] * rs; sh[t] = b4[t] - m * sc[t];
+        }
+        __syncthreads();
+        for (int item = t; item < 512; item += 256) {
+            int b = item >> 7, oc = item & 127;
+            float s = sc[oc], h = sh[oc];
+            float mx = 0.f;
+#pragma unroll
+            for (int k = 0; k < 16; k++) mx = fmaxf(mx, g_h4[(b * 16 + k) * 128 + oc] * s + h);
+            pooled[b * 128 + oc] = mx;
+        }
+        __syncthreads();
+        if (t < 20) {
+            int b = t / 5, cls = t % 5;
+            float acc = fcb[cls];
+            const float* w = &fcw[cls * 128];
+            for (int oc = 0; oc < 128; oc++) acc += pooled[b * 128 + oc] * w[oc];
+            out[b * 5 + cls] = acc;
+        }
     }
 }
 
@@ -570,10 +619,6 @@
     const float* fcw = (const float*)d_in[16]; const float* fcb = (const float*)d_in[17];
     float* out = (float*)d_out;
 
-    k_prep <<<dim3(128), dim3(256), 0, stream>>>(srn_w, w2, w3, w4);
-    k_srn  <<<dim3(240), dim3(256), 0, stream>>>(x);
-    k_conv2<<<dim3(224), dim3(256), 0, stream>>>(g1, b1);
-    k_conv3<<<dim3(96),  dim3(256), 0, stream>>>(g2, b2);
-    k_conv4<<<dim3(128), dim3(256), 0, stream>>>(g3, b3);
-    k_final<<<dim3(1),   dim3(256), 0, stream>>>(g4, b4, fcw, fcb, out);
+    k_fused<<<dim3(GRID), dim3(256), 62976, stream>>>(
+        x, srn_w, w2, w3, w4, g1, b1, g2, b2, g3, b3, g4, b4, fcw, fcb, out);
 }
```

New measurement: 354.8 us. 207% more time.
